# Kernel optimization log

Hardware: AMD Instinct MI355X
Metric: run time of the kernel (lower is better)

The kernel has to match this reference:

```python
import jax, jax.numpy as jnp
import numpy as np
from jax import lax

# Static problem configuration (SAModule(ratio=0.25, r=0.2, MLP([35,64,64,128])))
B, N, C_IN = 8, 4096, 32
RATIO, R, K = 0.25, 0.2, 64   # K == max_num_neighbors
M = int(N * RATIO)            # centroids per cloud after FPS
NEG = -1e10


def setup_inputs() -> dict:
    key = jax.random.key(0)
    ks = jax.random.split(key, 6)
    x = jax.random.normal(ks[0], (B * N, C_IN), jnp.float32)
    pos = jax.random.uniform(ks[1], (B * N, 3), jnp.float32)  # unit cube -> r=0.2 balls are non-trivial
    batch = jnp.repeat(jnp.arange(B, dtype=jnp.int32), N)
    def lin(k, fan_in, fan_out):
        return jax.random.normal(k, (fan_in, fan_out), jnp.float32) * (1.0 / np.sqrt(fan_in))
    W1 = lin(ks[2], C_IN + 3, 64); b1 = jnp.zeros((64,), jnp.float32)
    W2 = lin(ks[3], 64, 64);       b2 = jnp.zeros((64,), jnp.float32)
    W3 = lin(ks[4], 64, 128);      b3 = jnp.zeros((128,), jnp.float32)
    return {"x": x, "pos": pos, "batch": batch,
            "W1": W1, "b1": b1, "W2": W2, "b2": b2, "W3": W3, "b3": b3}


def _fps_one(p):
    """Farthest-point sampling on one cloud p:[N,3] -> idx:[M] (deterministic start at 0)."""
    def body(carry, _):
        dmin, last = carry
        d = jnp.sum((p - p[last]) ** 2, axis=-1)         # [N] sq-dist to last picked point
        dmin = jnp.minimum(dmin, d)
        nxt = jnp.argmax(dmin).astype(jnp.int32)
        return (dmin, nxt), nxt
    init = (jnp.full((N,), 1e10, jnp.float32), jnp.int32(0))
    _, rest = lax.scan(body, init, None, length=M - 1)
    return jnp.concatenate([jnp.zeros((1,), jnp.int32), rest])


def _sa_one(p, xb, ib, W1, b1, W2, b2, W3, b3):
    """Radius ball-query + PointNetConv (gather -> MLP -> masked scatter-max) on one cloud."""
    ctr = p[ib]                                              # [M,3] sampled centroids
    d2 = jnp.sum((ctr[:, None, :] - p[None, :, :]) ** 2, -1)  # [M,N]
    negd, nbr = lax.top_k(-d2, K)                            # K nearest per centroid
    valid = (-negd) <= R * R                                 # inside-ball mask [M,K]
    xj = xb[nbr]                                             # [M,K,C_IN] gathered features
    rel = p[nbr] - ctr[:, None, :]                           # [M,K,3] relative positions
    h = jnp.concatenate([xj, rel], axis=-1)                  # message input [x_j, pos_j - pos_i]
    h = jax.nn.relu(h @ W1 + b1)
    h = jax.nn.relu(h @ W2 + b2)
    h = h @ W3 + b3                                          # plain last layer (PyG MLP plain_last)
    h = jnp.where(valid[..., None], h, NEG)
    return jnp.max(h, axis=1)                                # max aggregation -> [M,128]


def reference(x, pos, batch, W1, b1, W2, b2, W3, b3):
    pos3 = pos.reshape(B, N, 3)
    x3 = x.reshape(B, N, C_IN)
    idx = jax.vmap(_fps_one)(pos3)                           # [B,M]
    conv = lambda p, xb, ib: _sa_one(p, xb, ib, W1, b1, W2, b2, W3, b3)
    x_out = jax.vmap(conv)(pos3, x3, idx)                    # [B,M,128]
    pos_out = jnp.take_along_axis(pos3, idx[..., None], axis=1)  # [B,M,3]
    batch_out = jnp.repeat(jnp.arange(B, dtype=batch.dtype), M)
    return x_out.reshape(B * M, -1), pos_out.reshape(B * M, 3), batch_out
```

## Files before the change

### kernel.cpp

```cpp
#include <hip/hip_runtime.h>
#include <hip/hip_bf16.h>

#define BB 8
#define NN 4096
#define CIN 32
#define MM 1024
#define KNB 64
#define CAND 1024
#define FPS_T 256
#define FPS_PPT 16
#define ROWS 72

typedef __attribute__((ext_vector_type(8))) short  short8;
typedef __attribute__((ext_vector_type(4))) float  f32x4;
typedef __attribute__((ext_vector_type(2))) float  f32x2;

__device__ __forceinline__ float sq3(float dx, float dy, float dz) {
    return __fadd_rn(__fadd_rn(__fmul_rn(dx, dx), __fmul_rn(dy, dy)), __fmul_rn(dz, dz));
}

__device__ __forceinline__ unsigned short f2bf(float v) {
    union { __hip_bfloat16 b; unsigned short u; } cv;
    cv.b = __float2bfloat16(v);
    return cv.u;
}
__device__ __forceinline__ float bf2f(unsigned short u) {
    union { unsigned short u; __hip_bfloat16 b; } cv;
    cv.u = u;
    return __bfloat162float(cv.b);
}

static __device__ __forceinline__ f32x4 mfma16(short8 a, short8 b, f32x4 c) {
    return __builtin_amdgcn_mfma_f32_16x16x32_bf16(a, b, c, 0, 0, 0);
}

template<int CTRL>
__device__ __forceinline__ unsigned long long dpp_maxkey(unsigned long long k) {
    unsigned int lo = (unsigned int)k;
    unsigned int hi = (unsigned int)(k >> 32);
    unsigned int nlo = (unsigned int)__builtin_amdgcn_update_dpp((int)lo, (int)lo, CTRL, 0xF, 0xF, false);
    unsigned int nhi = (unsigned int)__builtin_amdgcn_update_dpp((int)hi, (int)hi, CTRL, 0xF, 0xF, false);
    unsigned long long nk = ((unsigned long long)nhi << 32) | (unsigned long long)nlo;
    return nk > k ? nk : k;
}

__global__ __launch_bounds__(256) void prep_kernel(
    const float* __restrict__ W1, const float* __restrict__ W2,
    const float* __restrict__ W3, unsigned short* __restrict__ wf)
{
    int gid = blockIdx.x * 256 + threadIdx.x;
    const float* W; int K, Ncol, base, slot;
    if (gid < 1024)      { W = W1; K = 35; Ncol = 64;  base = 0;     slot = gid; }
    else if (gid < 2048) { W = W2; K = 64; Ncol = 64;  base = 8192;  slot = gid - 1024; }
    else                 { W = W3; K = 64; Ncol = 128; base = 16384; slot = gid - 2048; }
    int lane = slot & 63, h = (slot >> 6) & 1, kstep = (slot >> 7) & 1, tile = slot >> 8;
    int col = tile * 16 + (lane & 15), quad = lane >> 4;
#pragma unroll
    for (int j = 0; j < 8; ++j) {
        int k = kstep * 32 + quad * 8 + j;
        float wv = (k < K) ? W[k * Ncol + col] : 0.0f;
        unsigned short hi = f2bf(wv);
        unsigned short v = h ? f2bf(wv - bf2f(hi)) : hi;
        wf[base + slot * 8 + j] = v;
    }
}

__global__ __launch_bounds__(FPS_T) void fps_kernel(
    const float* __restrict__ pos, int* __restrict__ idx_ws, float* __restrict__ out)
{
    const int b = blockIdx.x;
    const int t = threadIdx.x;
    __shared__ float4 plds4[NN];
    __shared__ int    chosen[MM];
    __shared__ __align__(16) unsigned long long part[2][FPS_T / 64];

    const float* P = pos + (size_t)b * NN * 3;
    for (int i = t; i < NN; i += FPS_T) {
        float4 v;
        v.x = P[3 * i]; v.y = P[3 * i + 1]; v.z = P[3 * i + 2]; v.w = 0.0f;
        plds4[i] = v;
    }
    if (t == 0) chosen[0] = 0;
    __syncthreads();

    f32x2 pxv[8], pyv[8], pzv[8], dminv[8];
#pragma unroll
    for (int s = 0; s < 8; ++s) {
        float4 a = plds4[t + 512 * s];
        float4 c = plds4[t + 512 * s + 256];
        pxv[s] = (f32x2){a.x, c.x};
        pyv[s] = (f32x2){a.y, c.y};
        pzv[s] = (f32x2){a.z, c.z};
        dminv[s] = (f32x2){1e10f, 1e10f};
    }

    int win = 0;
    for (int it = 1; it < MM; ++it) {
        float4 wc = plds4[win];
        const f32x2 lxv = (f32x2){wc.x, wc.x};
        const f32x2 lyv = (f32x2){wc.y, wc.y};
        const f32x2 lzv = (f32x2){wc.z, wc.z};
        float bv = -1.0f;
        int   bi = 0;
#pragma unroll
        for (int s = 0; s < 8; ++s) {
            f32x2 d;
            {
#pragma clang fp contract(off)
                f32x2 dx = pxv[s] - lxv;
                f32x2 dy = pyv[s] - lyv;
                f32x2 dz = pzv[s] - lzv;
                d = dx * dx + dy * dy + dz * dz;
            }
            float m0 = fminf(dminv[s].x, d.x);
            float m1 = fminf(dminv[s].y, d.y);
            dminv[s].x = m0;
            dminv[s].y = m1;
            if (m0 > bv) { bv = m0; bi = t + 512 * s; }
            if (m1 > bv) { bv = m1; bi = t + 512 * s + 256; }
        }
        unsigned long long k =
            ((unsigned long long)__float_as_uint(bv) << 32) | (unsigned int)(~bi);
        k = dpp_maxkey<0x111>(k);
        k = dpp_maxkey<0x112>(k);
        k = dpp_maxkey<0x114>(k);
        k = dpp_maxkey<0x118>(k);
        k = dpp_maxkey<0x142>(k);
        k = dpp_maxkey<0x143>(k);
        if ((t & 63) == 63) part[it & 1][t >> 6] = k;
        __syncthreads();
        const ulonglong2* pp = (const ulonglong2*)&part[it & 1][0];
        ulonglong2 p01 = pp[0], p23 = pp[1];
        unsigned long long ka = p01.x > p01.y ? p01.x : p01.y;
        unsigned long long kb = p23.x > p23.y ? p23.x : p23.y;
        unsigned long long km = ka > kb ? ka : kb;
        win = (int)(~(unsigned int)km);
        if (t == 0) chosen[it] = win;
    }
    __syncthreads();

    for (int m = t; m < MM; m += FPS_T) {
        int mi = chosen[m];
        idx_ws[b * MM + m] = mi;
        const int PO = BB * MM * 128;
        const int BO = PO + BB * MM * 3;
        int row = b * MM + m;
        float4 c = plds4[mi];
        out[PO + 3 * row + 0] = c.x;
        out[PO + 3 * row + 1] = c.y;
        out[PO + 3 * row + 2] = c.z;
        out[BO + row] = (float)b;
    }
}

__global__ __launch_bounds__(256, 4) void sa_kernel(
    const float* __restrict__ x, const float* __restrict__ pos,
    const int* __restrict__ idx_ws, const unsigned short* __restrict__ wf,
    const float* __restrict__ b1, const float* __restrict__ b2,
    const float* __restrict__ b3, float* __restrict__ out)
{
    const int bm = blockIdx.x;
    const int b  = bm >> 10;
    const int t  = threadIdx.x;
    const int w    = t >> 6;
    const int lane = t & 63;

    __shared__ unsigned short HA[2 * 64 * ROWS];
    __shared__ unsigned long long candk[CAND];
    __shared__ int   cnt;
    __shared__ int   sel[KNB];
    __shared__ float red[4][128];

    const float R2 = (float)(0.2 * 0.2);
    const float* P = pos + (size_t)b * NN * 3;
    const int ci = idx_ws[bm];

    if (t == 0) cnt = 0;
    __syncthreads();

    const float cx = P[3 * ci], cy = P[3 * ci + 1], cz = P[3 * ci + 2];

    for (int i = t; i < NN; i += 256) {
        float dx = P[3 * i] - cx, dy = P[3 * i + 1] - cy, dz = P[3 * i + 2] - cz;
        float d2 = sq3(dx, dy, dz);
        bool hit = d2 <= R2;
        unsigned long long m = __ballot(hit);
        if (m) {
            int leader = __ffsll((unsigned long long)m) - 1;
            int base = 0;
            if (lane == leader) base = atomicAdd(&cnt, __popcll(m));
            base = __shfl(base, leader);
            if (hit) {
                int p = base + __popcll(m & ((1ull << lane) - 1));
                if (p < CAND)
                    candk[p] = ((unsigned long long)__float_as_uint(d2) << 32)
                             | (unsigned int)i;
            }
        }
    }
    __syncthreads();
    const int n = min(cnt, CAND);
    const int V = min(n, KNB);

    for (int i = t; i < n; i += 256) {
        unsigned long long ki = candk[i];
        int rank = 0;
        for (int j = 0; j < n; ++j)
            rank += (candk[j] < ki) ? 1 : 0;
        if (rank < KNB) sel[rank] = (int)(ki & 0xffffffffu);
    }
    __syncthreads();

    {
        const int row = 16 * w + (lane & 15);
        const int prt = lane >> 4;
        short8 z = {};
        *(short8*)(HA + row * ROWS + 32 + prt * 8) = z;
        *(short8*)(HA + 64 * ROWS + row * ROWS + 32 + prt * 8) = z;
        if (row < V) {
            int g = b * NN + sel[row];
            const float4* xr = (const float4*)(x + (size_t)g * CIN + prt * 8);
            float4 v0 = xr[0], v1 = xr[1];
            float vv[8] = {v0.x, v0.y, v0.z, v0.w, v1.x, v1.y, v1.z, v1.w};
            short8 hv, lv;
#pragma unroll
            for (int j = 0; j < 8; ++j) {
                unsigned short h = f2bf(vv[j]);
                hv[j] = (short)h;
                lv[j] = (short)f2bf(vv[j] - bf2f(h));
            }
            *(short8*)(HA + row * ROWS + prt * 8) = hv;
            *(short8*)(HA + 64 * ROWS + row * ROWS + prt * 8) = lv;
            if (prt == 0) {
                int g2 = sel[row];
#pragma unroll
                for (int c = 0; c < 3; ++c) {
                    float cc = (c == 0) ? cx : (c == 1) ? cy : cz;
                    float rv = P[3 * g2 + c] - cc;
                    unsigned short h = f2bf(rv);
                    HA[row * ROWS + 32 + c] = h;
                    HA[64 * ROWS + row * ROWS + 32 + c] = f2bf(rv - bf2f(h));
                }
            }
        }
    }

    const int m16  = lane & 15;
    const int quad = lane >> 4;
    const int arow = 16 * w + m16;
    const short8* wf8 = (const short8*)wf;

    {
        short8 aH[2], aL[2];
        aH[0] = *(const short8*)(HA + arow * ROWS + quad * 8);
        aH[1] = *(const short8*)(HA + arow * ROWS + 32 + quad * 8);
        aL[0] = *(const short8*)(HA + 64 * ROWS + arow * ROWS + quad * 8);
        aL[1] = *(const short8*)(HA + 64 * ROWS + arow * ROWS + 32 + quad * 8);
#pragma unroll
        for (int tile = 0; tile < 4; ++tile) {
            f32x4 acc = {};
#pragma unroll
            for (int ks = 0; ks < 2; ++ks) {
                short8 bH = wf8[((tile * 2 + ks) * 2 + 0) * 64 + lane];
                short8 bL = wf8[((tile * 2 + ks) * 2 + 1) * 64 + lane];
                acc = mfma16(aH[ks], bH, acc);
                acc = mfma16(aH[ks], bL, acc);
                acc = mfma16(aL[ks], bH, acc);
            }
            int col = tile * 16 + m16;
            float bb = b1[col];
#pragma unroll
            for (int i = 0; i < 4; ++i) {
                int grow = 16 * w + quad * 4 + i;
                float v = fmaxf(acc[i] + bb, 0.0f);
                unsigned short h = f2bf(v);
                HA[grow * ROWS + col] = h;
                HA[64 * ROWS + grow * ROWS + col] = f2bf(v - bf2f(h));
            }
        }
    }

    {
        short8 aH[2], aL[2];
        aH[0] = *(const short8*)(HA + arow * ROWS + quad * 8);
        aH[1] = *(const short8*)(HA + arow * ROWS + 32 + quad * 8);
        aL[0] = *(const short8*)(HA + 64 * ROWS + arow * ROWS + quad * 8);
        aL[1] = *(const short8*)(HA + 64 * ROWS + arow * ROWS + 32 + quad * 8);
#pragma unroll
        for (int tile = 0; tile < 4; ++tile) {
            f32x4 acc = {};
#pragma unroll
            for (int ks = 0; ks < 2; ++ks) {
                short8 bH = wf8[1024 + ((tile * 2 + ks) * 2 + 0) * 64 + lane];
                short8 bL = wf8[1024 + ((tile * 2 + ks) * 2 + 1) * 64 + lane];
                acc = mfma16(aH[ks], bH, acc);
                acc = mfma16(aH[ks], bL, acc);
                acc = mfma16(aL[ks], bH, acc);
            }
            int col = tile * 16 + m16;
            float bb = b2[col];
#pragma unroll
            for (int i = 0; i < 4; ++i) {
                int grow = 16 * w + quad * 4 + i;
                float v = fmaxf(acc[i] + bb, 0.0f);
                unsigned short h = f2bf(v);
                HA[grow * ROWS + col] = h;
                HA[64 * ROWS + grow * ROWS + col] = f2bf(v - bf2f(h));
            }
        }
    }

    {
        short8 aH[2], aL[2];
        aH[0] = *(const short8*)(HA + arow * ROWS + quad * 8);
        aH[1] = *(const short8*)(HA + arow * ROWS + 32 + quad * 8);
        aL[0] = *(const short8*)(HA + 64 * ROWS + arow * ROWS + quad * 8);
        aL[1] = *(const short8*)(HA + 64 * ROWS + arow * ROWS + 32 + quad * 8);
#pragma unroll
        for (int tile = 0; tile < 8; ++tile) {
            f32x4 acc = {};
#pragma unroll
            for (int ks = 0; ks < 2; ++ks) {
                short8 bH = wf8[2048 + ((tile * 2 + ks) * 2 + 0) * 64 + lane];
                short8 bL = wf8[2048 + ((tile * 2 + ks) * 2 + 1) * 64 + lane];
                acc = mfma16(aH[ks], bH, acc);
                acc = mfma16(aH[ks], bL, acc);
                acc = mfma16(aL[ks], bH, acc);
            }
            float mv = -1e10f;
#pragma unroll
            for (int i = 0; i < 4; ++i) {
                int grow = 16 * w + quad * 4 + i;
                float v = (grow < V) ? acc[i] : -1e10f;
                mv = fmaxf(mv, v);
            }
            mv = fmaxf(mv, __shfl_xor(mv, 16));
            mv = fmaxf(mv, __shfl_xor(mv, 32));
            if (lane < 16) red[w][tile * 16 + lane] = mv;
        }
    }
    __syncthreads();

    if (t < 128) {
        float v = fmaxf(fmaxf(red[0][t], red[1][t]), fmaxf(red[2][t], red[3][t]));
        out[(size_t)bm * 128 + t] = v + b3[t];
    }
}

extern "C" void kernel_launch(void* const* d_in, const int* in_sizes, int n_in,
                              void* d_out, int out_size, void* d_ws, size_t ws_size,
                              hipStream_t stream) {
    const float* x   = (const float*)d_in[0];
    const float* pos = (const float*)d_in[1];
    const float* W1 = (const float*)d_in[3];
    const float* b1 = (const float*)d_in[4];
    const float* W2 = (const float*)d_in[5];
    const float* b2 = (const float*)d_in[6];
    const float* W3 = (const float*)d_in[7];
    const float* b3 = (const float*)d_in[8];
    float* out    = (float*)d_out;
    int*   idx_ws = (int*)d_ws;
    unsigned short* wf = (unsigned short*)((char*)d_ws + 32768);

    hipLaunchKernelGGL(prep_kernel, dim3(16), dim3(256), 0, stream, W1, W2, W3, wf);
    hipLaunchKernelGGL(fps_kernel, dim3(BB), dim3(FPS_T), 0, stream, pos, idx_ws, out);
    hipLaunchKernelGGL(sa_kernel, dim3(BB * MM), dim3(256), 0, stream,
                       x, pos, idx_ws, wf, b1, b2, b3, out);
}
```

Before: 793.6 us.

## Stream FPS picks to SA kernel via per-batch ready flags

FPS now writes each chosen index to global memory as soon as it is picked and publishes a per-batch progress counter every 64 picks with release semantics. The SA blocks spin-wait on that counter with acquire loads, so in principle they could start ball-query and MLP work before FPS finishes. Launch order is changed so FPS runs before weight prep, a memset clears the flags, and a dead-code path forces extra LDS use in the FPS kernel. Because all kernels are still on one stream, the SA kernel cannot actually run at the same time as FPS. The change therefore mostly adds a memset, per-iteration global stores and spin checks.

New measurement: 812.9 us. 1.02x slower.

```diff
diff --git a/kernel.cpp b/kernel.cpp
--- a/kernel.cpp
+++ b/kernel.cpp
@@ -8,7 +8,6 @@
 #define KNB 64
 #define CAND 1024
 #define FPS_T 256
-#define FPS_PPT 16
 #define ROWS 72
 
 typedef __attribute__((ext_vector_type(8))) short  short8;
@@ -66,13 +65,15 @@
 }
 
 __global__ __launch_bounds__(FPS_T) void fps_kernel(
-    const float* __restrict__ pos, int* __restrict__ idx_ws, float* __restrict__ out)
+    const float* __restrict__ pos, int* __restrict__ idx_ws,
+    unsigned int* __restrict__ ready, float* __restrict__ out)
 {
     const int b = blockIdx.x;
     const int t = threadIdx.x;
     __shared__ float4 plds4[NN];
     __shared__ int    chosen[MM];
     __shared__ __align__(16) unsigned long long part[2][FPS_T / 64];
+    __shared__ float4 lds_pad[4096];
 
     const float* P = pos + (size_t)b * NN * 3;
     for (int i = t; i < NN; i += FPS_T) {
@@ -80,7 +81,7 @@
         v.x = P[3 * i]; v.y = P[3 * i + 1]; v.z = P[3 * i + 2]; v.w = 0.0f;
         plds4[i] = v;
     }
-    if (t == 0) chosen[0] = 0;
+    if (t == 0) { chosen[0] = 0; idx_ws[b * MM] = 0; }
     __syncthreads();
 
     f32x2 pxv[8], pyv[8], pzv[8], dminv[8];
@@ -135,13 +136,18 @@
         unsigned long long kb = p23.x > p23.y ? p23.x : p23.y;
         unsigned long long km = ka > kb ? ka : kb;
         win = (int)(~(unsigned int)km);
-        if (t == 0) chosen[it] = win;
+        if (t == 0) {
+            chosen[it] = win;
+            idx_ws[b * MM + it] = win;
+            if ((it & 63) == 63)
+                __hip_atomic_store(&ready[b], (unsigned int)(it + 1),
+                                   __ATOMIC_RELEASE, __HIP_MEMORY_SCOPE_AGENT);
+        }
     }
     __syncthreads();
 
     for (int m = t; m < MM; m += FPS_T) {
         int mi = chosen[m];
-        idx_ws[b * MM + m] = mi;
         const int PO = BB * MM * 128;
         const int BO = PO + BB * MM * 3;
         int row = b * MM + m;
@@ -151,11 +157,16 @@
         out[PO + 3 * row + 2] = c.z;
         out[BO + row] = (float)b;
     }
+    if (chosen[0] != 0) {
+        lds_pad[t] = plds4[t];
+        out[t] = lds_pad[t].x;
+    }
 }
 
 __global__ __launch_bounds__(256, 4) void sa_kernel(
     const float* __restrict__ x, const float* __restrict__ pos,
-    const int* __restrict__ idx_ws, const unsigned short* __restrict__ wf,
+    const int* __restrict__ idx_ws, const unsigned int* __restrict__ ready,
+    const unsigned short* __restrict__ wf,
     const float* __restrict__ b1, const float* __restrict__ b2,
     const float* __restrict__ b3, float* __restrict__ out)
 {
@@ -173,11 +184,17 @@
 
     const float R2 = (float)(0.2 * 0.2);
     const float* P = pos + (size_t)b * NN * 3;
+
+    const unsigned int need = (unsigned int)((bm & (MM - 1)) + 1);
+    if (t == 0) {
+        while (__hip_atomic_load(&ready[b], __ATOMIC_ACQUIRE,
+                                 __HIP_MEMORY_SCOPE_AGENT) < need)
+            __builtin_amdgcn_s_sleep(2);
+        cnt = 0;
+    }
+    __syncthreads();
+
     const int ci = idx_ws[bm];
-
-    if (t == 0) cnt = 0;
-    __syncthreads();
-
     const float cx = P[3 * ci], cy = P[3 * ci + 1], cz = P[3 * ci + 2];
 
     for (int i = t; i < NN; i += 256) {
@@ -361,9 +378,12 @@
     float* out    = (float*)d_out;
     int*   idx_ws = (int*)d_ws;
     unsigned short* wf = (unsigned short*)((char*)d_ws + 32768);
-
+    unsigned int* ready = (unsigned int*)((char*)d_ws + 81920);
+
+    hipMemsetAsync(ready, 0, BB * sizeof(unsigned int), stream);
+    hipLaunchKernelGGL(fps_kernel, dim3(BB), dim3(FPS_T), 0, stream,
+                       pos, idx_ws, ready, out);
     hipLaunchKernelGGL(prep_kernel, dim3(16), dim3(256), 0, stream, W1, W2, W3, wf);
-    hipLaunchKernelGGL(fps_kernel, dim3(BB), dim3(FPS_T), 0, stream, pos, idx_ws, out);
     hipLaunchKernelGGL(sa_kernel, dim3(BB * MM), dim3(256), 0, stream,
-                       x, pos, idx_ws, wf, b1, b2, b3, out);
-}
+                       x, pos, idx_ws, ready, wf, b1, b2, b3, out);
+}
```

## Fuse FPS and SA into persistent kernel with producer-consumer overlap

Applied to the files above, without the earlier changes.

Merges farthest-point sampling and the set-abstraction MLP into one persistent kernel. Eight high-priority blocks run FPS and publish chosen indices plus a ready counter every 32 iterations, while the remaining blocks poll the counter and process centroids as soon as they are available, overlapping the serial FPS with the SA work. A bounded spin budget with a fallback sweep kernel, driven by per-row done flags, covers items that timed out. The aim is to hide the long serial FPS latency behind SA compute, at the cost of spin-waiting, cross-block memory ordering, an extra memset, and a second launch.

Result: faster. 707.9 us, median of 2 (-10.8%).

```diff
diff --git a/kernel.cpp b/kernel.cpp
--- a/kernel.cpp
+++ b/kernel.cpp
@@ -7,9 +7,9 @@
 #define MM 1024
 #define KNB 64
 #define CAND 1024
-#define FPS_T 256
-#define FPS_PPT 16
 #define ROWS 72
+#define GRID 256
+#define NWORK (GRID - 8)
 
 typedef __attribute__((ext_vector_type(8))) short  short8;
 typedef __attribute__((ext_vector_type(4))) float  f32x4;
@@ -65,117 +65,27 @@
     }
 }
 
-__global__ __launch_bounds__(FPS_T) void fps_kernel(
-    const float* __restrict__ pos, int* __restrict__ idx_ws, float* __restrict__ out)
+struct SaShared {
+    unsigned short HA[2 * 64 * ROWS];
+    unsigned long long candk[CAND];
+    int   cnt;
+    int   ok;
+    int   sel[KNB];
+    float red[4][128];
+};
+
+__device__ __forceinline__ void sa_process(
+    SaShared& sh, const float* __restrict__ x, const float* __restrict__ P,
+    const unsigned short* __restrict__ wf,
+    const float* __restrict__ b1, const float* __restrict__ b2,
+    const float* __restrict__ b3, float* __restrict__ out, int bm, int b, int ci)
 {
-    const int b = blockIdx.x;
-    const int t = threadIdx.x;
-    __shared__ float4 plds4[NN];
-    __shared__ int    chosen[MM];
-    __shared__ __align__(16) unsigned long long part[2][FPS_T / 64];
-
-    const float* P = pos + (size_t)b * NN * 3;
-    for (int i = t; i < NN; i += FPS_T) {
-        float4 v;
-        v.x = P[3 * i]; v.y = P[3 * i + 1]; v.z = P[3 * i + 2]; v.w = 0.0f;
-        plds4[i] = v;
-    }
-    if (t == 0) chosen[0] = 0;
-    __syncthreads();
-
-    f32x2 pxv[8], pyv[8], pzv[8], dminv[8];
-#pragma unroll
-    for (int s = 0; s < 8; ++s) {
-        float4 a = plds4[t + 512 * s];
-        float4 c = plds4[t + 512 * s + 256];
-        pxv[s] = (f32x2){a.x, c.x};
-        pyv[s] = (f32x2){a.y, c.y};
-        pzv[s] = (f32x2){a.z, c.z};
-        dminv[s] = (f32x2){1e10f, 1e10f};
-    }
-
-    int win = 0;
-    for (int it = 1; it < MM; ++it) {
-        float4 wc = plds4[win];
-        const f32x2 lxv = (f32x2){wc.x, wc.x};
-        const f32x2 lyv = (f32x2){wc.y, wc.y};
-        const f32x2 lzv = (f32x2){wc.z, wc.z};
-        float bv = -1.0f;
-        int   bi = 0;
-#pragma unroll
-        for (int s = 0; s < 8; ++s) {
-            f32x2 d;
-            {
-#pragma clang fp contract(off)
-                f32x2 dx = pxv[s] - lxv;
-                f32x2 dy = pyv[s] - lyv;
-                f32x2 dz = pzv[s] - lzv;
-                d = dx * dx + dy * dy + dz * dz;
-            }
-            float m0 = fminf(dminv[s].x, d.x);
-            float m1 = fminf(dminv[s].y, d.y);
-            dminv[s].x = m0;
-            dminv[s].y = m1;
-            if (m0 > bv) { bv = m0; bi = t + 512 * s; }
-            if (m1 > bv) { bv = m1; bi = t + 512 * s + 256; }
-        }
-        unsigned long long k =
-            ((unsigned long long)__float_as_uint(bv) << 32) | (unsigned int)(~bi);
-        k = dpp_maxkey<0x111>(k);
-        k = dpp_maxkey<0x112>(k);
-        k = dpp_maxkey<0x114>(k);
-        k = dpp_maxkey<0x118>(k);
-        k = dpp_maxkey<0x142>(k);
-        k = dpp_maxkey<0x143>(k);
-        if ((t & 63) == 63) part[it & 1][t >> 6] = k;
-        __syncthreads();
-        const ulonglong2* pp = (const ulonglong2*)&part[it & 1][0];
-        ulonglong2 p01 = pp[0], p23 = pp[1];
-        unsigned long long ka = p01.x > p01.y ? p01.x : p01.y;
-        unsigned long long kb = p23.x > p23.y ? p23.x : p23.y;
-        unsigned long long km = ka > kb ? ka : kb;
-        win = (int)(~(unsigned int)km);
-        if (t == 0) chosen[it] = win;
-    }
-    __syncthreads();
-
-    for (int m = t; m < MM; m += FPS_T) {
-        int mi = chosen[m];
-        idx_ws[b * MM + m] = mi;
-        const int PO = BB * MM * 128;
-        const int BO = PO + BB * MM * 3;
-        int row = b * MM + m;
-        float4 c = plds4[mi];
-        out[PO + 3 * row + 0] = c.x;
-        out[PO + 3 * row + 1] = c.y;
-        out[PO + 3 * row + 2] = c.z;
-        out[BO + row] = (float)b;
-    }
-}
-
-__global__ __launch_bounds__(256, 4) void sa_kernel(
-    const float* __restrict__ x, const float* __restrict__ pos,
-    const int* __restrict__ idx_ws, const unsigned short* __restrict__ wf,
-    const float* __restrict__ b1, const float* __restrict__ b2,
-    const float* __restrict__ b3, float* __restrict__ out)
-{
-    const int bm = blockIdx.x;
-    const int b  = bm >> 10;
-    const int t  = threadIdx.x;
+    const int t    = threadIdx.x;
     const int w    = t >> 6;
     const int lane = t & 63;
-
-    __shared__ unsigned short HA[2 * 64 * ROWS];
-    __shared__ unsigned long long candk[CAND];
-    __shared__ int   cnt;
-    __shared__ int   sel[KNB];
-    __shared__ float red[4][128];
-
     const float R2 = (float)(0.2 * 0.2);
-    const float* P = pos + (size_t)b * NN * 3;
-    const int ci = idx_ws[bm];
-
-    if (t == 0) cnt = 0;
+
+    if (t == 0) sh.cnt = 0;
     __syncthreads();
 
     const float cx = P[3 * ci], cy = P[3 * ci + 1], cz = P[3 * ci + 2];
@@ -184,30 +94,30 @@
         float dx = P[3 * i] - cx, dy = P[3 * i + 1] - cy, dz = P[3 * i + 2] - cz;
         float d2 = sq3(dx, dy, dz);
         bool hit = d2 <= R2;
-        unsigned long long m = __ballot(hit);
-        if (m) {
-            int leader = __ffsll((unsigned long long)m) - 1;
+        unsigned long long mk = __ballot(hit);
+        if (mk) {
+            int leader = __ffsll((unsigned long long)mk) - 1;
             int base = 0;
-            if (lane == leader) base = atomicAdd(&cnt, __popcll(m));
+            if (lane == leader) base = atomicAdd(&sh.cnt, __popcll(mk));
             base = __shfl(base, leader);
             if (hit) {
-                int p = base + __popcll(m & ((1ull << lane) - 1));
+                int p = base + __popcll(mk & ((1ull << lane) - 1));
                 if (p < CAND)
-                    candk[p] = ((unsigned long long)__float_as_uint(d2) << 32)
-                             | (unsigned int)i;
+                    sh.candk[p] = ((unsigned long long)__float_as_uint(d2) << 32)
+                                | (unsigned int)i;
             }
         }
     }
     __syncthreads();
-    const int n = min(cnt, CAND);
+    const int n = min(sh.cnt, CAND);
     const int V = min(n, KNB);
 
     for (int i = t; i < n; i += 256) {
-        unsigned long long ki = candk[i];
+        unsigned long long ki = sh.candk[i];
         int rank = 0;
         for (int j = 0; j < n; ++j)
-            rank += (candk[j] < ki) ? 1 : 0;
-        if (rank < KNB) sel[rank] = (int)(ki & 0xffffffffu);
+            rank += (sh.candk[j] < ki) ? 1 : 0;
+        if (rank < KNB) sh.sel[rank] = (int)(ki & 0xffffffffu);
     }
     __syncthreads();
 
@@ -215,10 +125,10 @@
         const int row = 16 * w + (lane & 15);
         const int prt = lane >> 4;
         short8 z = {};
-        *(short8*)(HA + row * ROWS + 32 + prt * 8) = z;
-        *(short8*)(HA + 64 * ROWS + row * ROWS + 32 + prt * 8) = z;
+        *(short8*)(sh.HA + row * ROWS + 32 + prt * 8) = z;
+        *(short8*)(sh.HA + 64 * ROWS + row * ROWS + 32 + prt * 8) = z;
         if (row < V) {
-            int g = b * NN + sel[row];
+            int g = b * NN + sh.sel[row];
             const float4* xr = (const float4*)(x + (size_t)g * CIN + prt * 8);
             float4 v0 = xr[0], v1 = xr[1];
             float vv[8] = {v0.x, v0.y, v0.z, v0.w, v1.x, v1.y, v1.z, v1.w};
@@ -229,17 +139,17 @@
                 hv[j] = (short)h;
                 lv[j] = (short)f2bf(vv[j] - bf2f(h));
             }
-            *(short8*)(HA + row * ROWS + prt * 8) = hv;
-            *(short8*)(HA + 64 * ROWS + row * ROWS + prt * 8) = lv;
+            *(short8*)(sh.HA + row * ROWS + prt * 8) = hv;
+            *(short8*)(sh.HA + 64 * ROWS + row * ROWS + prt * 8) = lv;
             if (prt == 0) {
-                int g2 = sel[row];
+                int g2 = sh.sel[row];
 #pragma unroll
                 for (int c = 0; c < 3; ++c) {
                     float cc = (c == 0) ? cx : (c == 1) ? cy : cz;
                     float rv = P[3 * g2 + c] - cc;
                     unsigned short h = f2bf(rv);
-                    HA[row * ROWS + 32 + c] = h;
-                    HA[64 * ROWS + row * ROWS + 32 + c] = f2bf(rv - bf2f(h));
+                    sh.HA[row * ROWS + 32 + c] = h;
+                    sh.HA[64 * ROWS + row * ROWS + 32 + c] = f2bf(rv - bf2f(h));
                 }
             }
         }
@@ -252,10 +162,10 @@
 
     {
         short8 aH[2], aL[2];
-        aH[0] = *(const short8*)(HA + arow * ROWS + quad * 8);
-        aH[1] = *(const short8*)(HA + arow * ROWS + 32 + quad * 8);
-        aL[0] = *(const short8*)(HA + 64 * ROWS + arow * ROWS + quad * 8);
-        aL[1] = *(const short8*)(HA + 64 * ROWS + arow * ROWS + 32 + quad * 8);
+        aH[0] = *(const short8*)(sh.HA + arow * ROWS + quad * 8);
+        aH[1] = *(const short8*)(sh.HA + arow * ROWS + 32 + quad * 8);
+        aL[0] = *(const short8*)(sh.HA + 64 * ROWS + arow * ROWS + quad * 8);
+        aL[1] = *(const short8*)(sh.HA + 64 * ROWS + arow * ROWS + 32 + quad * 8);
 #pragma unroll
         for (int tile = 0; tile < 4; ++tile) {
             f32x4 acc = {};
@@ -274,18 +184,18 @@
                 int grow = 16 * w + quad * 4 + i;
                 float v = fmaxf(acc[i] + bb, 0.0f);
                 unsigned short h = f2bf(v);
-                HA[grow * ROWS + col] = h;
-                HA[64 * ROWS + grow * ROWS + col] = f2bf(v - bf2f(h));
+                sh.HA[grow * ROWS + col] = h;
+                sh.HA[64 * ROWS + grow * ROWS + col] = f2bf(v - bf2f(h));
             }
         }
     }
 
     {
         short8 aH[2], aL[2];
-        aH[0] = *(const short8*)(HA + arow * ROWS + quad * 8);
-        aH[1] = *(const short8*)(HA + arow * ROWS + 32 + quad * 8);
-        aL[0] = *(const short8*)(HA + 64 * ROWS + arow * ROWS + quad * 8);
-        aL[1] = *(const short8*)(HA + 64 * ROWS + arow * ROWS + 32 + quad * 8);
+        aH[0] = *(const short8*)(sh.HA + arow * ROWS + quad * 8);
+        aH[1] = *(const short8*)(sh.HA + arow * ROWS + 32 + quad * 8);
+        aL[0] = *(const short8*)(sh.HA + 64 * ROWS + arow * ROWS + quad * 8);
+        aL[1] = *(const short8*)(sh.HA + 64 * ROWS + arow * ROWS + 32 + quad * 8);
 #pragma unroll
         for (int tile = 0; tile < 4; ++tile) {
             f32x4 acc = {};
@@ -304,18 +214,18 @@
                 int grow = 16 * w + quad * 4 + i;
                 float v = fmaxf(acc[i] + bb, 0.0f);
                 unsigned short h = f2bf(v);
-                HA[grow * ROWS + col] = h;
-                HA[64 * ROWS + grow * ROWS + col] = f2bf(v - bf2f(h));
+                sh.HA[grow * ROWS + col] = h;
+                sh.HA[64 * ROWS + grow * ROWS + col] = f2bf(v - bf2f(h));
             }
         }
     }
 
     {
         short8 aH[2], aL[2];
-        aH[0] = *(const short8*)(HA + arow * ROWS + quad * 8);
-        aH[1] = *(const short8*)(HA + arow * ROWS + 32 + quad * 8);
-        aL[0] = *(const short8*)(HA + 64 * ROWS + arow * ROWS + quad * 8);
-        aL[1] = *(const short8*)(HA + 64 * ROWS + arow * ROWS + 32 + quad * 8);
+        aH[0] = *(const short8*)(sh.HA + arow * ROWS + quad * 8);
+        aH[1] = *(const short8*)(sh.HA + arow * ROWS + 32 + quad * 8);
+        aL[0] = *(const short8*)(sh.HA + 64 * ROWS + arow * ROWS + quad * 8);
+        aL[1] = *(const short8*)(sh.HA + 64 * ROWS + arow * ROWS + 32 + quad * 8);
 #pragma unroll
         for (int tile = 0; tile < 8; ++tile) {
             f32x4 acc = {};
@@ -336,15 +246,176 @@
             }
             mv = fmaxf(mv, __shfl_xor(mv, 16));
             mv = fmaxf(mv, __shfl_xor(mv, 32));
-            if (lane < 16) red[w][tile * 16 + lane] = mv;
+            if (lane < 16) sh.red[w][tile * 16 + lane] = mv;
         }
     }
     __syncthreads();
 
     if (t < 128) {
-        float v = fmaxf(fmaxf(red[0][t], red[1][t]), fmaxf(red[2][t], red[3][t]));
+        float v = fmaxf(fmaxf(sh.red[0][t], sh.red[1][t]),
+                        fmaxf(sh.red[2][t], sh.red[3][t]));
         out[(size_t)bm * 128 + t] = v + b3[t];
     }
+}
+
+union SharedMem {
+    struct {
+        float4 plds4[NN];
+        int    chosen[MM];
+        __align__(16) unsigned long long part[2][4];
+    } fps;
+    SaShared sa;
+};
+
+__global__ __launch_bounds__(256, 2) void fused_kernel(
+    const float* __restrict__ x, const float* __restrict__ pos,
+    int* __restrict__ idx_ws, unsigned int* __restrict__ ready,
+    int* __restrict__ done, const unsigned short* __restrict__ wf,
+    const float* __restrict__ b1, const float* __restrict__ b2,
+    const float* __restrict__ b3, float* __restrict__ out)
+{
+    __shared__ SharedMem sh;
+    const int t = threadIdx.x;
+
+    if (blockIdx.x < BB) {
+        __builtin_amdgcn_s_setprio(3);
+        const int b = blockIdx.x;
+        const float* P = pos + (size_t)b * NN * 3;
+        for (int i = t; i < NN; i += 256) {
+            float4 v;
+            v.x = P[3 * i]; v.y = P[3 * i + 1]; v.z = P[3 * i + 2]; v.w = 0.0f;
+            sh.fps.plds4[i] = v;
+        }
+        if (t == 0) {
+            sh.fps.chosen[0] = 0;
+            __hip_atomic_store(&idx_ws[b * MM], 0, __ATOMIC_RELAXED,
+                               __HIP_MEMORY_SCOPE_AGENT);
+        }
+        __syncthreads();
+
+        f32x2 pxv[8], pyv[8], pzv[8], dminv[8];
+#pragma unroll
+        for (int s = 0; s < 8; ++s) {
+            float4 a = sh.fps.plds4[t + 512 * s];
+            float4 c = sh.fps.plds4[t + 512 * s + 256];
+            pxv[s] = (f32x2){a.x, c.x};
+            pyv[s] = (f32x2){a.y, c.y};
+            pzv[s] = (f32x2){a.z, c.z};
+            dminv[s] = (f32x2){1e10f, 1e10f};
+        }
+
+        int win = 0;
+        for (int it = 1; it < MM; ++it) {
+            float4 wc = sh.fps.plds4[win];
+            const f32x2 lxv = (f32x2){wc.x, wc.x};
+            const f32x2 lyv = (f32x2){wc.y, wc.y};
+            const f32x2 lzv = (f32x2){wc.z, wc.z};
+            float bv = -1.0f;
+            int   bi = 0;
+#pragma unroll
+            for (int s = 0; s < 8; ++s) {
+                f32x2 d;
+                {
+#pragma clang fp contract(off)
+                    f32x2 dx = pxv[s] - lxv;
+                    f32x2 dy = pyv[s] - lyv;
+                    f32x2 dz = pzv[s] - lzv;
+                    d = dx * dx + dy * dy + dz * dz;
+                }
+                float m0 = fminf(dminv[s].x, d.x);
+                float m1 = fminf(dminv[s].y, d.y);
+                dminv[s].x = m0;
+                dminv[s].y = m1;
+                if (m0 > bv) { bv = m0; bi = t + 512 * s; }
+                if (m1 > bv) { bv = m1; bi = t + 512 * s + 256; }
+            }
+            unsigned long long k =
+                ((unsigned long long)__float_as_uint(bv) << 32) | (unsigned int)(~bi);
+            k = dpp_maxkey<0x111>(k);
+            k = dpp_maxkey<0x112>(k);
+            k = dpp_maxkey<0x114>(k);
+            k = dpp_maxkey<0x118>(k);
+            k = dpp_maxkey<0x142>(k);
+            k = dpp_maxkey<0x143>(k);
+            if ((t & 63) == 63) sh.fps.part[it & 1][t >> 6] = k;
+            __syncthreads();
+            const ulonglong2* pp = (const ulonglong2*)&sh.fps.part[it & 1][0];
+            ulonglong2 p01 = pp[0], p23 = pp[1];
+            unsigned long long ka = p01.x > p01.y ? p01.x : p01.y;
+            unsigned long long kb = p23.x > p23.y ? p23.x : p23.y;
+            unsigned long long km = ka > kb ? ka : kb;
+            win = (int)(~(unsigned int)km);
+            if (t == 0) {
+                sh.fps.chosen[it] = win;
+                __hip_atomic_store(&idx_ws[b * MM + it], win, __ATOMIC_RELAXED,
+                                   __HIP_MEMORY_SCOPE_AGENT);
+                if ((it & 31) == 31)
+                    __hip_atomic_store(&ready[b], (unsigned int)(it + 1),
+                                       __ATOMIC_RELEASE, __HIP_MEMORY_SCOPE_AGENT);
+            }
+        }
+        __syncthreads();
+
+        for (int m = t; m < MM; m += 256) {
+            int mi = sh.fps.chosen[m];
+            const int PO = BB * MM * 128;
+            const int BO = PO + BB * MM * 3;
+            int row = b * MM + m;
+            float4 c = sh.fps.plds4[mi];
+            out[PO + 3 * row + 0] = c.x;
+            out[PO + 3 * row + 1] = c.y;
+            out[PO + 3 * row + 2] = c.z;
+            out[BO + row] = (float)b;
+        }
+        return;
+    }
+
+    int budget = 8000;
+    for (int item = (int)blockIdx.x - BB; item < BB * MM; item += NWORK) {
+        const int m  = item >> 3;
+        const int b  = item & 7;
+        const int bm = b * MM + m;
+        const float* P = pos + (size_t)b * NN * 3;
+
+        if (t == 0) {
+            const unsigned int need = (unsigned int)(m + 1);
+            while (budget > 0 &&
+                   __hip_atomic_load(&ready[b], __ATOMIC_ACQUIRE,
+                                     __HIP_MEMORY_SCOPE_AGENT) < need) {
+                __builtin_amdgcn_s_sleep(10);
+                --budget;
+            }
+            sh.sa.ok = (__hip_atomic_load(&ready[b], __ATOMIC_ACQUIRE,
+                                          __HIP_MEMORY_SCOPE_AGENT) >= need) ? 1 : 0;
+        }
+        __syncthreads();
+        const int myok = sh.sa.ok;
+        __syncthreads();
+        if (!myok) continue;
+
+        const int ci = __hip_atomic_load(&idx_ws[bm], __ATOMIC_RELAXED,
+                                         __HIP_MEMORY_SCOPE_AGENT) & (NN - 1);
+        sa_process(sh.sa, x, P, wf, b1, b2, b3, out, bm, b, ci);
+        if (t == 0)
+            __hip_atomic_store(&done[bm], 1, __ATOMIC_RELAXED,
+                               __HIP_MEMORY_SCOPE_AGENT);
+    }
+}
+
+__global__ __launch_bounds__(256, 4) void sweep_kernel(
+    const float* __restrict__ x, const float* __restrict__ pos,
+    const int* __restrict__ idx_ws, const int* __restrict__ done,
+    const unsigned short* __restrict__ wf,
+    const float* __restrict__ b1, const float* __restrict__ b2,
+    const float* __restrict__ b3, float* __restrict__ out)
+{
+    __shared__ SaShared sh;
+    const int bm = blockIdx.x;
+    if (done[bm]) return;
+    const int b = bm >> 10;
+    const float* P = pos + (size_t)b * NN * 3;
+    const int ci = idx_ws[bm] & (NN - 1);
+    sa_process(sh, x, P, wf, b1, b2, b3, out, bm, b, ci);
 }
 
 extern "C" void kernel_launch(void* const* d_in, const int* in_sizes, int n_in,
@@ -361,9 +432,13 @@
     float* out    = (float*)d_out;
     int*   idx_ws = (int*)d_ws;
     unsigned short* wf = (unsigned short*)((char*)d_ws + 32768);
-
+    unsigned int* ready = (unsigned int*)((char*)d_ws + 98304);
+    int* done = (int*)((char*)d_ws + 98368);
+
+    hipMemsetAsync((char*)d_ws + 98304, 0, 131136 - 98304, stream);
     hipLaunchKernelGGL(prep_kernel, dim3(16), dim3(256), 0, stream, W1, W2, W3, wf);
-    hipLaunchKernelGGL(fps_kernel, dim3(BB), dim3(FPS_T), 0, stream, pos, idx_ws, out);
-    hipLaunchKernelGGL(sa_kernel, dim3(BB * MM), dim3(256), 0, stream,
-                       x, pos, idx_ws, wf, b1, b2, b3, out);
-}
+    hipLaunchKernelGGL(fused_kernel, dim3(GRID), dim3(256), 0, stream,
+                       x, pos, idx_ws, ready, done, wf, b1, b2, b3, out);
+    hipLaunchKernelGGL(sweep_kernel, dim3(BB * MM), dim3(256), 0, stream,
+                       x, pos, idx_ws, done, wf, b1, b2, b3, out);
+}
```
